# Optimization experiments

Measured on AMD Instinct MI355X. Metric: run time of the kernel, lower is better.

Reference implementation:

```python
import jax, jax.numpy as jnp
import numpy as np

B, C, H, W = 32, 512, 32, 32
R = C // 2  # reduced channels for key/prod projections


def setup_inputs() -> dict:
    key = jax.random.key(0)
    ks = jax.random.split(key, 8)
    s_in = 1.0 / np.sqrt(C)
    return {
        "x": jax.random.normal(ks[0], (B, C, H, W), jnp.float32),
        "Wk": jax.random.normal(ks[1], (R, C), jnp.float32) * s_in,
        "bk": jax.random.normal(ks[2], (R,), jnp.float32) * s_in,
        "Wp": jax.random.normal(ks[3], (R, C), jnp.float32) * s_in,
        "bp": jax.random.normal(ks[4], (R,), jnp.float32) * s_in,
        "Wv": jax.random.normal(ks[5], (C, C), jnp.float32) * s_in,
        "bv": jax.random.normal(ks[6], (C,), jnp.float32) * s_in,
        "param": jax.random.normal(ks[7], (1,), jnp.float32),
    }


def _conv1x1(x, Wmat, b):
    # 1x1 conv on NCHW == per-pixel channel matmul
    return jnp.einsum('bchw,oc->bohw', x, Wmat) + b[None, :, None, None]


def reference(x, Wk, bk, Wp, bp, Wv, bv, param):
    b, c, h, w = x.shape
    hw = h * w
    f_key = _conv1x1(x, Wk, bk).reshape(b, -1, hw).transpose(0, 2, 1)  # [B,HW,R]
    f_prod = _conv1x1(x, Wp, bp).reshape(b, -1, hw)                    # [B,R,HW]
    f_value = _conv1x1(x, Wv, bv).reshape(b, -1, hw)                   # [B,C,HW]
    energy = jnp.einsum('bnr,brm->bnm', f_key, f_prod)                 # [B,HW,HW]
    similarity = jax.nn.softmax(energy, axis=-1)
    # bmm(f_value, similarity^T): out[b,c,n] = sum_m f_value[b,c,m] * sim[b,n,m]
    attended = jnp.einsum('bcm,bnm->bcn', f_value, similarity).reshape(b, c, h, w)
    return x + attended * param
```

## Files before the change

kernel.cpp:

```cpp
#include <hip/hip_runtime.h>
#include <hip/hip_bf16.h>

#define BATCH 32
#define CCH   512
#define HWSZ  1024
#define RCH   256

typedef __attribute__((ext_vector_type(8))) _Float16 f16x8;
typedef __attribute__((ext_vector_type(4))) float f32x4;

__device__ __forceinline__ ushort f2h(float f) {
    _Float16 h = (_Float16)f;
    ushort u; __builtin_memcpy(&u, &h, 2);
    return u;
}
__device__ __forceinline__ float h2f(ushort u) {
    _Float16 h; __builtin_memcpy(&h, &u, 2);
    return (float)h;
}

__device__ __forceinline__ void load_lds16(const void* g, void* l) {
    __builtin_amdgcn_global_load_lds((const __attribute__((address_space(1))) void*)g,
                                     (__attribute__((address_space(3))) void*)l,
                                     16, 0, 0);
}

__device__ __forceinline__ void xcd_swizzle(int& bx, int& by, int& bz) {
    int gx = gridDim.x, gy = gridDim.y;
    int n   = gx * gy * gridDim.z;
    int lin = bx + gx * (by + gy * bz);
    int cpx = n >> 3;
    int s = (lin & 7) * cpx + (lin >> 3);
    bx = s % gx; s /= gx;
    by = s % gy;
    bz = s / gy;
}

__global__ __launch_bounds__(256) void k_prep_w(
    const float* __restrict__ Wk, const float* __restrict__ bk,
    const float* __restrict__ Wp, const float* __restrict__ bp,
    const float* __restrict__ Wv,
    ushort* __restrict__ Wkp_h, ushort* __restrict__ Wv_h, float* __restrict__ bias_kp)
{
    int idx = blockIdx.x * 256 + threadIdx.x;
    if (idx < 512 * 512) {
        int o = idx >> 9, c = idx & 511;
        float w = (o < 256) ? Wk[o * 512 + c] : Wp[(o - 256) * 512 + c];
        Wkp_h[idx] = f2h(w);
        Wv_h[idx]  = f2h(Wv[idx]);
        if (c == 0) bias_kp[o] = (o < 256) ? bk[o] : bp[o - 256];
    }
}

__global__ __launch_bounds__(256) void k_transpose(
    const float* __restrict__ x, ushort* __restrict__ xt)
{
    __shared__ float tile[64][65];
    int b  = blockIdx.z;
    int c0 = blockIdx.y * 64;
    int n0 = blockIdx.x * 64;
    const float* xb = x + (size_t)b * CCH * HWSZ;
    int t  = threadIdx.x;
    int tq = t >> 6;
    int tl = t & 63;
    #pragma unroll
    for (int i = 0; i < 16; ++i) {
        int c = i * 4 + tq;
        tile[c][tl] = xb[(size_t)(c0 + c) * HWSZ + n0 + tl];
    }
    __syncthreads();
    ushort* oh = xt + (size_t)b * HWSZ * CCH;
    #pragma unroll
    for (int i = 0; i < 16; ++i) {
        int n = i * 4 + tq;
        oh[(size_t)(n0 + n) * CCH + c0 + tl] = f2h(tile[tl][n]);
    }
}

template<int MODE>
__global__ __launch_bounds__(512, 2) void k_gemm8(
    const ushort* __restrict__ A, const ushort* __restrict__ B,
    int lda, int ldb, long aBatch, long bBatch,
    float* __restrict__ outF, ushort* __restrict__ out16,
    long oBatch, int ldo,
    const float* __restrict__ bias,
    const float* __restrict__ xres, const float* __restrict__ param,
    int NT)
{
    __shared__ ushort lds[2][2][2][8192];
    int bx = blockIdx.x, by = blockIdx.y, bz = blockIdx.z;
    xcd_swizzle(bx, by, bz);
    const int z  = bz;
    const int m0 = bx * 256;
    const int n0 = by * 256;
    const int t    = threadIdx.x;
    const int lane = t & 63;
    const int w    = t >> 6;
    const int wm = w >> 2, wn = w & 3;
    const int l15 = lane & 15;
    const int G   = (lane >> 4) ^ ((lane >> 1) & 3);

    const ushort* Ab = A + (size_t)z * aBatch;
    const ushort* Bb = B + (size_t)z * bBatch;

    const int sr = t >> 2;
    const int sg = (t & 3) ^ ((t >> 3) & 3);

    f32x4 acc[8][4] = {};
    f16x8 a[8], b[2];

#define STAGE(par, op, ks, kt) do {                                          \
        const ushort* gb_ = (op) ? Bb : Ab;                                  \
        int ld_ = (op) ? ldb : lda;                                          \
        int r0_ = (op) ? n0 : m0;                                            \
        size_t src_ = (size_t)(r0_ + sr) * ld_ + (kt) * 64 + (ks) * 32 + sg * 8; \
        load_lds16(gb_ + src_, &lds[par][op][ks][t * 8]);                    \
        load_lds16(gb_ + src_ + (size_t)128 * ld_, &lds[par][op][ks][t * 8 + 4096]); \
    } while (0)

#define LDA_(cur, ks) do {                                                   \
        _Pragma("unroll")                                                    \
        for (int mi = 0; mi < 8; ++mi)                                       \
            a[mi] = *(const f16x8*)&lds[cur][0][ks][(wm * 128 + mi * 16 + l15) * 32 + G * 8]; \
    } while (0)

#define LDB_(cur, ks, nh) do {                                               \
        _Pragma("unroll")                                                    \
        for (int ni = 0; ni < 2; ++ni)                                       \
            b[ni] = *(const f16x8*)&lds[cur][1][ks][(wn * 64 + (nh) * 32 + ni * 16 + l15) * 32 + G * 8]; \
    } while (0)

#define BAR() __builtin_amdgcn_s_barrier()

#define MFMA_BLK(nh) do {                                                    \
        asm volatile("s_waitcnt lgkmcnt(0)" ::: "memory");                   \
        __builtin_amdgcn_sched_barrier(0);                                   \
        __builtin_amdgcn_s_setprio(1);                                       \
        _Pragma("unroll")                                                    \
        for (int mi = 0; mi < 8; ++mi) {                                     \
            acc[mi][(nh)*2+0] = __builtin_amdgcn_mfma_f32_16x16x32_f16(a[mi], b[0], acc[mi][(nh)*2+0], 0, 0, 0); \
            acc[mi][(nh)*2+1] = __builtin_amdgcn_mfma_f32_16x16x32_f16(a[mi], b[1], acc[mi][(nh)*2+1], 0, 0, 0); \
        }                                                                    \
        __builtin_amdgcn_s_setprio(0);                                       \
    } while (0)

    STAGE(0, 0, 0, 0); STAGE(0, 1, 0, 0); STAGE(0, 0, 1, 0); STAGE(0, 1, 1, 0);
    asm volatile("s_waitcnt vmcnt(4)" ::: "memory");
    BAR();

    for (int j = 0; j < NT - 1; ++j) {
        int cur = j & 1, nxt = cur ^ 1;
        STAGE(nxt, 0, 0, j + 1);
        LDA_(cur, 0); LDB_(cur, 0, 0);
        BAR();
        MFMA_BLK(0);
        BAR();
        STAGE(nxt, 1, 0, j + 1);
        LDB_(cur, 0, 1);
        BAR();
        MFMA_BLK(1);
        asm volatile("s_waitcnt vmcnt(4)" ::: "memory");
        BAR();
        STAGE(nxt, 0, 1, j + 1);
        LDA_(cur, 1); LDB_(cur, 1, 0);
        BAR();
        MFMA_BLK(0);
        BAR();
        STAGE(nxt, 1, 1, j + 1);
        LDB_(cur, 1, 1);
        BAR();
        MFMA_BLK(1);
        asm volatile("s_waitcnt vmcnt(4)" ::: "memory");
        BAR();
    }
    {
        int cur = (NT - 1) & 1;
        LDA_(cur, 0); LDB_(cur, 0, 0);
        BAR();
        MFMA_BLK(0);
        BAR();
        LDB_(cur, 0, 1);
        BAR();
        MFMA_BLK(1);
        asm volatile("s_waitcnt vmcnt(0)" ::: "memory");
        BAR();
        LDA_(cur, 1); LDB_(cur, 1, 0);
        BAR();
        MFMA_BLK(0);
        BAR();
        LDB_(cur, 1, 1);
        BAR();
        MFMA_BLK(1);
    }

    const float prm = (MODE == 3) ? param[0] : 0.f;
    #pragma unroll
    for (int mi = 0; mi < 8; ++mi) {
        #pragma unroll
        for (int ni = 0; ni < 4; ++ni) {
            int gc  = n0 + wn * 64 + (ni >> 1) * 32 + (ni & 1) * 16 + l15;
            int gr0 = m0 + wm * 128 + mi * 16 + (lane >> 4) * 4;
            if (MODE == 3) {
                float*       ob = outF + (size_t)z * oBatch;
                const float* xb = xres + (size_t)z * oBatch;
                size_t g = (size_t)gc * ldo + gr0;
                float4 xv = *(const float4*)&xb[g];
                float4 ov;
                ov.x = xv.x + acc[mi][ni][0] * prm;
                ov.y = xv.y + acc[mi][ni][1] * prm;
                ov.z = xv.z + acc[mi][ni][2] * prm;
                ov.w = xv.w + acc[mi][ni][3] * prm;
                *(float4*)&ob[g] = ov;
            } else {
                #pragma unroll
                for (int jj = 0; jj < 4; ++jj) {
                    int gr = gr0 + jj;
                    float v = acc[mi][ni][jj];
                    if (MODE == 0) {
                        v += bias[gc];
                        out16[(size_t)gr * ldo + gc] = f2h(v);
                    } else if (MODE == 1) {
                        v += bias[gr];
                        out16[(size_t)z * oBatch + (size_t)gr * ldo + gc] = f2h(v);
                    } else {
                        out16[(size_t)z * oBatch + (size_t)gr * ldo + gc] = f2h(v);
                    }
                }
            }
        }
    }
#undef STAGE
#undef LDA_
#undef LDB_
#undef BAR
#undef MFMA_BLK
}

__global__ __launch_bounds__(256) void k_softmax(ushort* __restrict__ E)
{
    int blk = blockIdx.x;
    ushort* row = E + (size_t)blk * HWSZ;
    int t = threadIdx.x;
    ushort4 u = *(const ushort4*)&row[t * 4];
    float v0 = h2f(u.x), v1 = h2f(u.y), v2 = h2f(u.z), v3 = h2f(u.w);
    float mx = fmaxf(fmaxf(v0, v1), fmaxf(v2, v3));
    #pragma unroll
    for (int off = 1; off < 64; off <<= 1)
        mx = fmaxf(mx, __shfl_xor(mx, off));
    __shared__ float redm[4];
    __shared__ float reds[4];
    int lane = t & 63, wv = t >> 6;
    if (lane == 0) redm[wv] = mx;
    __syncthreads();
    mx = fmaxf(fmaxf(redm[0], redm[1]), fmaxf(redm[2], redm[3]));
    float e0 = __expf(v0 - mx), e1 = __expf(v1 - mx);
    float e2 = __expf(v2 - mx), e3 = __expf(v3 - mx);
    float s = (e0 + e1) + (e2 + e3);
    #pragma unroll
    for (int off = 1; off < 64; off <<= 1)
        s += __shfl_xor(s, off);
    if (lane == 0) reds[wv] = s;
    __syncthreads();
    s = (reds[0] + reds[1]) + (reds[2] + reds[3]);
    float inv = 1.0f / s;
    ushort4 o;
    o.x = f2h(e0 * inv); o.y = f2h(e1 * inv);
    o.z = f2h(e2 * inv); o.w = f2h(e3 * inv);
    *(ushort4*)&row[t * 4] = o;
}

extern "C" void kernel_launch(void* const* d_in, const int* in_sizes, int n_in,
                              void* d_out, int out_size, void* d_ws, size_t ws_size,
                              hipStream_t stream)
{
    const float* x    = (const float*)d_in[0];
    const float* Wk   = (const float*)d_in[1];
    const float* bk   = (const float*)d_in[2];
    const float* Wp   = (const float*)d_in[3];
    const float* bp   = (const float*)d_in[4];
    const float* Wv   = (const float*)d_in[5];
    const float* bv   = (const float*)d_in[6];
    const float* prm  = (const float*)d_in[7];
    float* out = (float*)d_out;
    char* ws = (char*)d_ws;

    const size_t SZ16 = (size_t)BATCH * HWSZ * CCH * 2;
    ushort* xt    = (ushort*)(ws + 0);
    ushort* KPt   = (ushort*)(ws + SZ16);
    ushort* fv    = (ushort*)(ws + 2 * SZ16);
    ushort* E     = (ushort*)(ws + 3 * SZ16);
    char* wbase   = ws + 3 * SZ16 + (size_t)BATCH * HWSZ * HWSZ * 2;
    ushort* Wkp_h = (ushort*)(wbase);
    ushort* Wv_h  = (ushort*)(wbase + 524288);
    float*  bias_kp = (float*)(wbase + 2 * 524288);

    k_prep_w<<<1024, 256, 0, stream>>>(Wk, bk, Wp, bp, Wv, Wkp_h, Wv_h, bias_kp);
    k_transpose<<<dim3(16, 8, 32), 256, 0, stream>>>(x, xt);

    k_gemm8<0><<<dim3(128, 2, 1), 512, 0, stream>>>(
        xt, Wkp_h, CCH, CCH, 0, 0,
        nullptr, KPt, 0, CCH,
        bias_kp, nullptr, nullptr, CCH / 64);

    k_gemm8<1><<<dim3(2, 4, 32), 512, 0, stream>>>(
        Wv_h, xt, CCH, CCH, 0, (long)HWSZ * CCH,
        nullptr, fv, (long)CCH * HWSZ, HWSZ,
        bv, nullptr, nullptr, CCH / 64);

    k_gemm8<2><<<dim3(4, 4, 32), 512, 0, stream>>>(
        KPt, KPt + RCH, CCH, CCH,
        (long)HWSZ * CCH, (long)HWSZ * CCH,
        nullptr, E, (long)HWSZ * HWSZ, HWSZ,
        nullptr, nullptr, nullptr, RCH / 64);

    k_softmax<<<BATCH * HWSZ, 256, 0, stream>>>(E);

    k_gemm8<3><<<dim3(4, 2, 32), 512, 0, stream>>>(
        E, fv, HWSZ, HWSZ,
        (long)HWSZ * HWSZ, (long)CCH * HWSZ,
        out, nullptr, (long)CCH * HWSZ, HWSZ,
        nullptr, x, prm, HWSZ / 64);
}
```

Measured before the change: 196.8 us.

## Fuse softmax into energy GEMM epilogue and apply row scaling in output GEMM

Removes the standalone softmax kernel. The energy GEMM now computes per-256-column-tile row max and exp-sum in its epilogue, stores exp(energy - local max) as fp16, and writes per-tile (max, sum) stats to workspace. The output GEMM merges the four tile stats per row into per-tile scale factors and multiplies the A fragments by them with packed fp16 multiplies before the MFMAs. This drops a full read-modify-write pass over the B×HW×HW fp16 energy matrix, at the cost of extra LDS, epilogue shuffles, and launch bounds reduced to one block per CU.

```diff
diff --git a/kernel.cpp b/kernel.cpp
--- a/kernel.cpp
+++ b/kernel.cpp
@@ -13,10 +13,6 @@
     _Float16 h = (_Float16)f;
     ushort u; __builtin_memcpy(&u, &h, 2);
     return u;
-}
-__device__ __forceinline__ float h2f(ushort u) {
-    _Float16 h; __builtin_memcpy(&h, &u, 2);
-    return (float)h;
 }
 
 __device__ __forceinline__ void load_lds16(const void* g, void* l) {
@@ -78,7 +74,7 @@
 }
 
 template<int MODE>
-__global__ __launch_bounds__(512, 2) void k_gemm8(
+__global__ __launch_bounds__(512, 1) void k_gemm8(
     const ushort* __restrict__ A, const ushort* __restrict__ B,
     int lda, int ldb, long aBatch, long bBatch,
     float* __restrict__ outF, ushort* __restrict__ out16,
@@ -88,6 +84,9 @@
     int NT)
 {
     __shared__ ushort lds[2][2][2][8192];
+    __shared__ float  pstat[256][4];
+    __shared__ float  mrow[256];
+    __shared__ ushort sctab[256][4];
     int bx = blockIdx.x, by = blockIdx.y, bz = blockIdx.z;
     xcd_swizzle(bx, by, bz);
     const int z  = bz;
@@ -98,7 +97,8 @@
     const int w    = t >> 6;
     const int wm = w >> 2, wn = w & 3;
     const int l15 = lane & 15;
-    const int G   = (lane >> 4) ^ ((lane >> 1) & 3);
+    const int hi  = lane >> 4;
+    const int G   = hi ^ ((lane >> 1) & 3);
 
     const ushort* Ab = A + (size_t)z * aBatch;
     const ushort* Bb = B + (size_t)z * bBatch;
@@ -108,6 +108,21 @@
 
     f32x4 acc[8][4] = {};
     f16x8 a[8], b[2];
+    uint2 scq[8];
+
+    if (MODE == 3) {
+        if (t < 256) {
+            const float* gs = bias + ((size_t)z * 1024 + m0 + t) * 8;
+            float4 s01 = *(const float4*)gs;
+            float4 s23 = *(const float4*)(gs + 4);
+            float mg = fmaxf(fmaxf(s01.x, s01.z), fmaxf(s23.x, s23.z));
+            float e0 = __expf(s01.x - mg), e1 = __expf(s01.z - mg);
+            float e2 = __expf(s23.x - mg), e3 = __expf(s23.z - mg);
+            float inv = 1.0f / (e0 * s01.y + e1 * s01.w + e2 * s23.y + e3 * s23.w);
+            sctab[t][0] = f2h(e0 * inv); sctab[t][1] = f2h(e1 * inv);
+            sctab[t][2] = f2h(e2 * inv); sctab[t][3] = f2h(e3 * inv);
+        }
+    }
 
 #define STAGE(par, op, ks, kt) do {                                          \
         const ushort* gb_ = (op) ? Bb : Ab;                                  \
@@ -132,9 +147,24 @@
 
 #define BAR() __builtin_amdgcn_s_barrier()
 
+#define XFORM() do {                                                         \
+        int q_ = jq >> 2;                                                    \
+        _Pragma("unroll")                                                    \
+        for (int mi = 0; mi < 8; ++mi) {                                     \
+            unsigned u_ = (q_ & 2) ? scq[mi].y : scq[mi].x;                  \
+            unsigned h_ = (q_ & 1) ? (u_ >> 16) : (u_ & 0xffffu);            \
+            unsigned ss_ = h_ * 0x10001u;                                    \
+            unsigned* ap_ = (unsigned*)&a[mi];                               \
+            _Pragma("unroll")                                                \
+            for (int k_ = 0; k_ < 4; ++k_)                                   \
+                asm("v_pk_mul_f16 %0, %0, %1" : "+v"(ap_[k_]) : "v"(ss_));   \
+        }                                                                    \
+    } while (0)
+
 #define MFMA_BLK(nh) do {                                                    \
         asm volatile("s_waitcnt lgkmcnt(0)" ::: "memory");                   \
         __builtin_amdgcn_sched_barrier(0);                                   \
+        if (MODE == 3 && (nh) == 0) XFORM();                                 \
         __builtin_amdgcn_s_setprio(1);                                       \
         _Pragma("unroll")                                                    \
         for (int mi = 0; mi < 8; ++mi) {                                     \
@@ -145,11 +175,17 @@
     } while (0)
 
     STAGE(0, 0, 0, 0); STAGE(0, 1, 0, 0); STAGE(0, 0, 1, 0); STAGE(0, 1, 1, 0);
-    asm volatile("s_waitcnt vmcnt(4)" ::: "memory");
+    asm volatile("s_waitcnt vmcnt(4) lgkmcnt(0)" ::: "memory");
     BAR();
+    if (MODE == 3) {
+        #pragma unroll
+        for (int mi = 0; mi < 8; ++mi)
+            scq[mi] = *(const uint2*)&sctab[wm * 128 + mi * 16 + l15][0];
+    }
 
     for (int j = 0; j < NT - 1; ++j) {
         int cur = j & 1, nxt = cur ^ 1;
+        int jq = j;
         STAGE(nxt, 0, 0, j + 1);
         LDA_(cur, 0); LDB_(cur, 0, 0);
         BAR();
@@ -175,6 +211,7 @@
     }
     {
         int cur = (NT - 1) & 1;
+        int jq = NT - 1;
         LDA_(cur, 0); LDB_(cur, 0, 0);
         BAR();
         MFMA_BLK(0);
@@ -191,6 +228,51 @@
         LDB_(cur, 1, 1);
         BAR();
         MFMA_BLK(1);
+    }
+
+    if (MODE == 2) {
+        #pragma unroll
+        for (int mi = 0; mi < 8; ++mi)
+            #pragma unroll
+            for (int jj = 0; jj < 4; ++jj) {
+                float v = fmaxf(fmaxf(acc[mi][0][jj], acc[mi][1][jj]),
+                                fmaxf(acc[mi][2][jj], acc[mi][3][jj]));
+                #pragma unroll
+                for (int off = 1; off < 16; off <<= 1)
+                    v = fmaxf(v, __shfl_xor(v, off));
+                if (l15 == 0) pstat[wm * 128 + mi * 16 + hi * 4 + jj][wn] = v;
+            }
+        __syncthreads();
+        if (t < 256) {
+            float4 p4 = *(const float4*)pstat[t];
+            mrow[t] = fmaxf(fmaxf(p4.x, p4.y), fmaxf(p4.z, p4.w));
+        }
+        __syncthreads();
+        #pragma unroll
+        for (int mi = 0; mi < 8; ++mi)
+            #pragma unroll
+            for (int jj = 0; jj < 4; ++jj) {
+                float m_ = mrow[wm * 128 + mi * 16 + hi * 4 + jj];
+                float s_ = 0.f;
+                #pragma unroll
+                for (int ni = 0; ni < 4; ++ni) {
+                    float p = __expf(acc[mi][ni][jj] - m_);
+                    acc[mi][ni][jj] = p;
+                    s_ += p;
+                }
+                #pragma unroll
+                for (int off = 1; off < 16; off <<= 1)
+                    s_ += __shfl_xor(s_, off);
+                if (l15 == 0) pstat[wm * 128 + mi * 16 + hi * 4 + jj][wn] = s_;
+            }
+        __syncthreads();
+        if (t < 256) {
+            float4 p4 = *(const float4*)pstat[t];
+            float2 st;
+            st.x = mrow[t];
+            st.y = (p4.x + p4.y) + (p4.z + p4.w);
+            *(float2*)&outF[((size_t)z * 1024 + m0 + t) * 8 + (size_t)(n0 >> 8) * 2] = st;
+        }
     }
 
     const float prm = (MODE == 3) ? param[0] : 0.f;
@@ -199,7 +281,7 @@
         #pragma unroll
         for (int ni = 0; ni < 4; ++ni) {
             int gc  = n0 + wn * 64 + (ni >> 1) * 32 + (ni & 1) * 16 + l15;
-            int gr0 = m0 + wm * 128 + mi * 16 + (lane >> 4) * 4;
+            int gr0 = m0 + wm * 128 + mi * 16 + hi * 4;
             if (MODE == 3) {
                 float*       ob = outF + (size_t)z * oBatch;
                 const float* xb = xres + (size_t)z * oBatch;
@@ -233,40 +315,8 @@
 #undef LDA_
 #undef LDB_
 #undef BAR
+#undef XFORM
 #undef MFMA_BLK
-}
-
-__global__ __launch_bounds__(256) void k_softmax(ushort* __restrict__ E)
-{
-    int blk = blockIdx.x;
-    ushort* row = E + (size_t)blk * HWSZ;
-    int t = threadIdx.x;
-    ushort4 u = *(const ushort4*)&row[t * 4];
-    float v0 = h2f(u.x), v1 = h2f(u.y), v2 = h2f(u.z), v3 = h2f(u.w);
-    float mx = fmaxf(fmaxf(v0, v1), fmaxf(v2, v3));
-    #pragma unroll
-    for (int off = 1; off < 64; off <<= 1)
-        mx = fmaxf(mx, __shfl_xor(mx, off));
-    __shared__ float redm[4];
-    __shared__ float reds[4];
-    int lane = t & 63, wv = t >> 6;
-    if (lane == 0) redm[wv] = mx;
-    __syncthreads();
-    mx = fmaxf(fmaxf(redm[0], redm[1]), fmaxf(redm[2], redm[3]));
-    float e0 = __expf(v0 - mx), e1 = __expf(v1 - mx);
-    float e2 = __expf(v2 - mx), e3 = __expf(v3 - mx);
-    float s = (e0 + e1) + (e2 + e3);
-    #pragma unroll
-    for (int off = 1; off < 64; off <<= 1)
-        s += __shfl_xor(s, off);
-    if (lane == 0) reds[wv] = s;
-    __syncthreads();
-    s = (reds[0] + reds[1]) + (reds[2] + reds[3]);
-    float inv = 1.0f / s;
-    ushort4 o;
-    o.x = f2h(e0 * inv); o.y = f2h(e1 * inv);
-    o.z = f2h(e2 * inv); o.w = f2h(e3 * inv);
-    *(ushort4*)&row[t * 4] = o;
 }
 
 extern "C" void kernel_launch(void* const* d_in, const int* in_sizes, int n_in,
@@ -293,6 +343,7 @@
     ushort* Wkp_h = (ushort*)(wbase);
     ushort* Wv_h  = (ushort*)(wbase + 524288);
     float*  bias_kp = (float*)(wbase + 2 * 524288);
+    float*  gstats  = (float*)(wbase + 3 * 524288);
 
     k_prep_w<<<1024, 256, 0, stream>>>(Wk, bk, Wp, bp, Wv, Wkp_h, Wv_h, bias_kp);
     k_transpose<<<dim3(16, 8, 32), 256, 0, stream>>>(x, xt);
@@ -310,14 +361,12 @@
     k_gemm8<2><<<dim3(4, 4, 32), 512, 0, stream>>>(
         KPt, KPt + RCH, CCH, CCH,
         (long)HWSZ * CCH, (long)HWSZ * CCH,
-        nullptr, E, (long)HWSZ * HWSZ, HWSZ,
+        gstats, E, (long)HWSZ * HWSZ, HWSZ,
         nullptr, nullptr, nullptr, RCH / 64);
-
-    k_softmax<<<BATCH * HWSZ, 256, 0, stream>>>(E);
 
     k_gemm8<3><<<dim3(4, 2, 32), 512, 0, stream>>>(
         E, fv, HWSZ, HWSZ,
         (long)HWSZ * HWSZ, (long)CCH * HWSZ,
         out, nullptr, (long)CCH * HWSZ, HWSZ,
-        nullptr, x, prm, HWSZ / 64);
-}
+        gstats, x, prm, HWSZ / 64);
+}
```

Result: slower. 211.0 us (+7.3%).
